# Kernel tuning notes

Hardware: AMD Instinct MI355X
Metric: run time of the kernel (lower is better)

## Reference

```python
import jax, jax.numpy as jnp
from jax import lax
import numpy as np

N_VOX = 50000
B = 2
D, H, W = 8, 160, 160
CIN = 16
G = 3
K = 27
CHANS = [(16, 16), (16, 32), (32, 64), (64, 64), (64, 128)]
NAMES = ['in', 'e1', 'e2', 'e3', 'out']


def setup_inputs() -> dict:
    key = jax.random.key(0)
    ks = jax.random.split(key, 16)
    rng = np.random.default_rng(0)
    # unique active cells -> deterministic scatter/gather rulebook
    lin = rng.choice(B * D * H * W, size=N_VOX, replace=False)
    bz = lin // (D * H * W)
    rem = lin % (D * H * W)
    zz = rem // (H * W)
    yy = (rem % (H * W)) // W
    xx = rem % W
    coors = jnp.asarray(np.stack([bz, zz, yy, xx], 1).astype(np.int32))
    inp = {
        'voxel_features': jax.random.normal(ks[0], (N_VOX, CIN), jnp.float32),
        'coors': coors,
        'batch_size': B,
    }
    i = 1
    for nm, (ci, co) in zip(NAMES, CHANS):
        k1, k2 = jax.random.split(ks[i]); i += 1
        inp['wb_' + nm] = jax.random.normal(k1, (K, ci, co), jnp.float32) * 0.05
        inp['ws_' + nm] = jax.random.normal(k2, (K, ci, G, co), jnp.float32) * 0.05
        inp['gm_' + nm] = jnp.ones((co,), jnp.float32)
        inp['bt_' + nm] = jnp.zeros((co,), jnp.float32)
    return inp


def _kan_block(feat, nbr, wb, ws, gm, bt, centers, inv_h):
    # submanifold KAN conv: gather -> (silu base + RBF spline basis) GEMM -> accumulate
    n = feat.shape[0]
    fp = jnp.concatenate([feat, jnp.zeros((1, feat.shape[1]), feat.dtype)], 0)  # pad row for out-of-grid

    def body(acc, kin):
        idx, wbk, wsk = kin
        x = fp[idx]                                   # [N, Cin] gathered neighbors
        base = jax.nn.silu(x) @ wbk                   # [N, Cout]
        bas = jnp.exp(-jnp.square((x[:, :, None] - centers) * inv_h))  # [N, Cin, G]
        spl = jnp.einsum('ncg,cgo->no', bas, wsk)     # [N, Cout]
        return acc + base + spl, None

    out0 = jnp.zeros((n, wb.shape[-1]), feat.dtype)
    out, _ = lax.scan(jax.checkpoint(body), out0, (nbr, wb, ws))
    # BatchNorm1d (train-mode batch stats) + ReLU
    mu = out.mean(0)
    var = out.var(0)
    out = (out - mu) * lax.rsqrt(var + 1e-3) * gm + bt
    return jax.nn.relu(out)


def _build_rulebook(coors, batch_size, n):
    grid = jnp.full((batch_size, D + 2, H + 2, W + 2), n, jnp.int32)
    grid = grid.at[coors[:, 0], coors[:, 1] + 1, coors[:, 2] + 1, coors[:, 3] + 1].set(
        jnp.arange(n, dtype=jnp.int32))
    offs = [(dz, dy, dx) for dz in (-1, 0, 1) for dy in (-1, 0, 1) for dx in (-1, 0, 1)]
    return jnp.stack([
        grid[coors[:, 0], coors[:, 1] + 1 + dz, coors[:, 2] + 1 + dy, coors[:, 3] + 1 + dx]
        for dz, dy, dx in offs])  # [27, N]


def reference(voxel_features, coors, batch_size,
              wb_in, ws_in, gm_in, bt_in,
              wb_e1, ws_e1, gm_e1, bt_e1,
              wb_e2, ws_e2, gm_e2, bt_e2,
              wb_e3, ws_e3, gm_e3, bt_e3,
              wb_out, ws_out, gm_out, bt_out):
    n = voxel_features.shape[0]
    nbr = _build_rulebook(coors, batch_size, n)
    centers = jnp.linspace(-1.0, 1.0, G)
    inv_h = (G - 1) / 2.0
    x = _kan_block(voxel_features, nbr, wb_in, ws_in, gm_in, bt_in, centers, inv_h)
    x = _kan_block(x, nbr, wb_e1, ws_e1, gm_e1, bt_e1, centers, inv_h)
    x = _kan_block(x, nbr, wb_e2, ws_e2, gm_e2, bt_e2, centers, inv_h)
    x = _kan_block(x, nbr, wb_e3, ws_e3, gm_e3, bt_e3, centers, inv_h)
    x = _kan_block(x, nbr, wb_out, ws_out, gm_out, bt_out, centers, inv_h)
    co = x.shape[1]
    dense = jnp.zeros((batch_size, D, H, W, co), x.dtype)
    dense = dense.at[coors[:, 0], coors[:, 1], coors[:, 2], coors[:, 3]].set(x)
    dense = dense.transpose(0, 4, 1, 2, 3)            # [B, C, D, H, W]
    return dense.reshape(batch_size, co * D, H, W)    # [B, C*D, H, W]
```

## Files before the change

### kernel.cpp

```cpp
#include <hip/hip_runtime.h>

#define N_VOX 50000
#define BATCH 2
#define DD 8
#define HH 160
#define WW 160
#define PD 10
#define PH 162
#define PW 162
#define KK 27
#define NCELL (BATCH*DD*HH*WW)
#define GRID_ELEMS (BATCH*PD*PH*PW)
#define OUT_ELEMS (BATCH*128*DD*HH*WW)

typedef __attribute__((ext_vector_type(8))) short short8v;
typedef __attribute__((ext_vector_type(4))) float float4v;

__device__ inline unsigned short f2bf(float f) {
    unsigned u = __float_as_uint(f);
    u += 0x7FFFu + ((u >> 16) & 1u);
    return (unsigned short)(u >> 16);
}

__global__ void k_flags(const int* __restrict__ coors, int* __restrict__ flags) {
    int n = blockIdx.x * 256 + threadIdx.x;
    if (n >= N_VOX) return;
    int b = coors[n*4+0], z = coors[n*4+1], y = coors[n*4+2], x = coors[n*4+3];
    flags[((b*DD + z)*HH + y)*WW + x] = 1;
}

__global__ void k_scan1(const int* __restrict__ flags, int* __restrict__ scanout,
                        int* __restrict__ bsums) {
    __shared__ int s[256];
    int t = threadIdx.x, blk = blockIdx.x;
    int4 v = ((const int4*)(flags + blk*1024))[t];
    int tsum = v.x + v.y + v.z + v.w;
    s[t] = tsum; __syncthreads();
    for (int off = 1; off < 256; off <<= 1) {
        int x = (t >= off) ? s[t-off] : 0;
        __syncthreads(); s[t] += x; __syncthreads();
    }
    int excl = s[t] - tsum;
    int4 o; o.x = excl; o.y = excl + v.x; o.z = o.y + v.y; o.w = o.z + v.z;
    ((int4*)(scanout + blk*1024))[t] = o;
    if (t == 255) bsums[blk] = s[255];
}

__global__ void k_scan2(int* __restrict__ bsums) {
    __shared__ int s[512];
    int t = threadIdx.x;
    int orig = (t < 400) ? bsums[t] : 0;
    s[t] = orig; __syncthreads();
    for (int off = 1; off < 512; off <<= 1) {
        int x = (t >= off) ? s[t-off] : 0;
        __syncthreads(); s[t] += x; __syncthreads();
    }
    if (t < 400) bsums[t] = s[t] - orig;
}

__global__ void k_pos(const int* __restrict__ coors, const int* __restrict__ scanout,
                      const int* __restrict__ bsums, int* __restrict__ pos_of,
                      int* __restrict__ vox_at) {
    int n = blockIdx.x * 256 + threadIdx.x;
    if (n >= N_VOX) return;
    int b = coors[n*4+0], z = coors[n*4+1], y = coors[n*4+2], x = coors[n*4+3];
    int lin = ((b*DD + z)*HH + y)*WW + x;
    int pos = scanout[lin] + bsums[lin >> 10];
    pos_of[n] = pos;
    vox_at[pos] = n;
}

__global__ void k_gridP(const int* __restrict__ coors, const int* __restrict__ pos_of,
                        int* __restrict__ gridP) {
    int n = blockIdx.x * 256 + threadIdx.x;
    if (n >= N_VOX) return;
    int b = coors[n*4+0], z = coors[n*4+1], y = coors[n*4+2], x = coors[n*4+3];
    gridP[((b*PD + z+1)*PH + (y+1))*PW + (x+1)] = pos_of[n];
}

__global__ void k_nbrP(const int* __restrict__ coors, const int* __restrict__ vox_at,
                       const int* __restrict__ gridP, int* __restrict__ nbrP) {
    int i = blockIdx.x * 256 + threadIdx.x;
    if (i >= N_VOX) return;
    int n = vox_at[i];
    int b = coors[n*4+0], z = coors[n*4+1]+1, y = coors[n*4+2]+1, x = coors[n*4+3]+1;
    int k = 0;
    for (int dz = -1; dz <= 1; ++dz)
        for (int dy = -1; dy <= 1; ++dy)
            for (int dx = -1; dx <= 1; ++dx) {
                int g = gridP[((b*PD + z+dz)*PH + (y+dy))*PW + (x+dx)];
                nbrP[k*N_VOX + i] = (g >= 0) ? g : N_VOX;
                ++k;
            }
}

__global__ void k_phi0(const float* __restrict__ vf, const int* __restrict__ vox_at,
                       unsigned short* __restrict__ phi) {
    int e = blockIdx.x * 256 + threadIdx.x;
    if (e >= (N_VOX + 1) * 16) return;
    int i = e / 16, c = e % 16;
    float x = 0.f;
    if (i < N_VOX) x = vf[(size_t)vox_at[i] * 16 + c];
    float sig = 1.f / (1.f + __expf(-x));
    ushort4 p;
    p.x = f2bf(x * sig);
    p.y = f2bf(__expf(-(x + 1.f) * (x + 1.f)));
    p.z = f2bf(__expf(-x * x));
    p.w = f2bf(__expf(-(x - 1.f) * (x - 1.f)));
    *(ushort4*)&phi[(size_t)e * 4] = p;
}

struct WswzArgs {
    const float* wb[5];
    const float* ws[5];
    unsigned short* dst[5];
};
__global__ void k_wswz_all(WswzArgs a) {
    constexpr int off[6]   = {0, 27648, 82944, 304128, 746496, 1631232};
    constexpr int lgCI4[5] = {6, 6, 7, 8, 8};
    constexpr int lgCO[5]  = {4, 5, 6, 6, 7};
    int e = blockIdx.x * 256 + threadIdx.x;
    if (e >= off[5]) return;
    int L = 0;
    #pragma unroll
    for (int i = 1; i < 5; ++i) L += (e >= off[i]);
    int el = e - off[L];
    int CIN4 = 1 << lgCI4[L], COUT = 1 << lgCO[L], CIN = CIN4 >> 2;
    int j8   = el & 7;
    int rest = el >> 3;
    int o    = rest & (COUT - 1);
    int kb   = rest >> lgCO[L];
    int kabs = kb * 8 + j8;
    int k  = kabs >> lgCI4[L];
    int c4 = kabs & (CIN4 - 1);
    int c = c4 >> 2, jj = c4 & 3;
    float v = (jj == 0) ? a.wb[L][(k * CIN + c) * COUT + o]
                        : a.ws[L][((k * CIN + c) * 3 + (jj - 1)) * COUT + o];
    a.dst[L][el] = f2bf(v);
}

template<int CIN, int COUT, int NSPL>
__global__ __launch_bounds__(64, 2) void k_conv_mfma(
    const unsigned short* __restrict__ phi,
    const int*            __restrict__ nbrP,
    const unsigned short* __restrict__ Wsw,
    float*                __restrict__ pre,
    float*                __restrict__ sums)
{
    constexpr int CIN4   = CIN * 4;
    constexpr int BK     = 64;
    constexpr int SPK    = CIN4 / BK;
    constexpr int NSTAGE = KK * SPK;
    constexpr int COUTH  = COUT / NSPL;
    constexpr int NFW    = COUTH / 16;
    constexpr int WR     = 4;
    constexpr int NMB    = (N_VOX + 63) / 64;
    constexpr int NBLK   = NMB * NSPL;
    constexpr int PERX   = (NBLK + 7) / 8;

    int lb = blockIdx.x;
    int linear = (lb & 7) * PERX + (lb >> 3);
    if (linear >= NBLK) return;
    const int mb = linear / NSPL, h = linear % NSPL;

    const int lane = threadIdx.x & 63;
    const int l15 = lane & 15, q = lane >> 4;
    const int base = mb * 64;
    int vg[WR];
    #pragma unroll
    for (int rs = 0; rs < WR; ++rs) vg[rs] = base + rs * 16 + l15;
    const int ob = h * COUTH;

    const unsigned short* bp = Wsw + (size_t)(q * COUT + ob + l15) * 8;

    int rows[WR], rowsN[WR];
    short8v A0[2][WR], A1[2][WR];
    short8v B0[2][NFW], B1[2][NFW];

    auto loadB = [&](int sp, short8v (&Bb)[2][NFW]) {
        #pragma unroll
        for (int kk = 0; kk < 2; ++kk)
            #pragma unroll
            for (int nf = 0; nf < NFW; ++nf)
                Bb[kk][nf] = *(const short8v*)(bp +
                    ((size_t)(sp * 8 + kk * 4) * COUT + nf * 16) * 8);
    };
    auto loadA = [&](int sp, short8v (&Ab)[2][WR]) {
        if (sp % SPK == 0) {
            #pragma unroll
            for (int rs = 0; rs < WR; ++rs) rows[rs] = rowsN[rs];
        }
        const int c4s = (sp % SPK) * BK;
        #pragma unroll
        for (int rs = 0; rs < WR; ++rs) {
            const unsigned short* p = phi + (size_t)rows[rs] * CIN4 + c4s + q * 8;
            Ab[0][rs] = *(const short8v*)p;
            Ab[1][rs] = *(const short8v*)(p + 32);
        }
        if (sp % SPK == 0) {
            int k2 = sp / SPK + 1;
            if (k2 < KK) {
                #pragma unroll
                for (int rs = 0; rs < WR; ++rs)
                    rowsN[rs] = (vg[rs] < N_VOX) ? nbrP[k2 * N_VOX + vg[rs]] : N_VOX;
            }
        }
    };

    float4v acc[WR][NFW];
    #pragma unroll
    for (int rs = 0; rs < WR; ++rs)
        #pragma unroll
        for (int nf = 0; nf < NFW; ++nf)
            acc[rs][nf] = (float4v){0.f, 0.f, 0.f, 0.f};

    auto domfma = [&](const short8v (&Ab)[2][WR], const short8v (&Bb)[2][NFW]) {
        #pragma unroll
        for (int kk = 0; kk < 2; ++kk)
            #pragma unroll
            for (int nf = 0; nf < NFW; ++nf)
                #pragma unroll
                for (int rs = 0; rs < WR; ++rs)
                    acc[rs][nf] = __builtin_amdgcn_mfma_f32_16x16x32_bf16(
                        Ab[kk][rs], Bb[kk][nf], acc[rs][nf], 0, 0, 0);
    };

    #pragma unroll
    for (int rs = 0; rs < WR; ++rs) {
        rows[rs]  = (vg[rs] < N_VOX) ? nbrP[vg[rs]] : N_VOX;
        rowsN[rs] = (vg[rs] < N_VOX) ? nbrP[N_VOX + vg[rs]] : N_VOX;
    }
    loadB(0, B0);
    #pragma unroll
    for (int rs = 0; rs < WR; ++rs) {
        const unsigned short* p = phi + (size_t)rows[rs] * CIN4 + q * 8;
        A0[0][rs] = *(const short8v*)p;
        A0[1][rs] = *(const short8v*)(p + 32);
    }

    #define SLOT(T, Ac, Bc, An, Bn)                                   \
        if ((T) + 1 < NSTAGE) { loadB((T) + 1, Bn); loadA((T) + 1, An); } \
        __builtin_amdgcn_sched_barrier(0);                            \
        domfma(Ac, Bc);

    int s = 0;
    for (; s + 2 <= NSTAGE; s += 2) {
        SLOT(s + 0, A0, B0, A1, B1)
        SLOT(s + 1, A1, B1, A0, B0)
    }
    if constexpr (NSTAGE % 2 != 0) {
        domfma(A0, B0);
    }
    #undef SLOT

    #pragma unroll
    for (int rs = 0; rs < WR; ++rs)
        #pragma unroll
        for (int nf = 0; nf < NFW; ++nf)
            #pragma unroll
            for (int r = 0; r < 4; ++r) {
                int v = base + rs * 16 + q * 4 + r;
                if (v < N_VOX)
                    pre[(size_t)v * COUT + ob + nf * 16 + l15] = acc[rs][nf][r];
            }

    float* S = sums + (blockIdx.x & 7) * 256;
    #pragma unroll
    for (int nf = 0; nf < NFW; ++nf) {
        float s1 = 0.f, s2 = 0.f;
        #pragma unroll
        for (int rs = 0; rs < WR; ++rs)
            #pragma unroll
            for (int r = 0; r < 4; ++r) {
                int v = base + rs * 16 + q * 4 + r;
                if (v < N_VOX) {
                    float a = acc[rs][nf][r];
                    s1 += a; s2 += a * a;
                }
            }
        s1 += __shfl_xor(s1, 16); s1 += __shfl_xor(s1, 32);
        s2 += __shfl_xor(s2, 16); s2 += __shfl_xor(s2, 32);
        if (q == 0) {
            atomicAdd(&S[ob + nf * 16 + l15], s1);
            atomicAdd(&S[COUT + ob + nf * 16 + l15], s2);
        }
    }
}

template<int COUT>
__global__ void k_bnapply_phi(const float* __restrict__ pre, const float* __restrict__ sums,
                              const float* __restrict__ gm, const float* __restrict__ bt,
                              unsigned short* __restrict__ phi) {
    __shared__ float sc[COUT], sh[COUT];
    int t = threadIdx.x;
    if (t < COUT) {
        float s1 = 0.f, s2 = 0.f;
        #pragma unroll
        for (int xo = 0; xo < 8; ++xo) {
            s1 += sums[xo * 256 + t];
            s2 += sums[xo * 256 + COUT + t];
        }
        float mu  = s1 * (1.f / N_VOX);
        float var = s2 * (1.f / N_VOX) - mu*mu;
        float s = rsqrtf(var + 1e-3f) * gm[t];
        sc[t] = s;
        sh[t] = bt[t] - mu * s;
    }
    __syncthreads();
    int tot = (N_VOX + 1) * COUT;
    for (int e = blockIdx.x*256 + t; e < tot; e += gridDim.x*256) {
        int i = e / COUT, c = e % COUT;
        float x = 0.f;
        if (i < N_VOX) x = fmaxf(pre[(size_t)i*COUT + c] * sc[c] + sh[c], 0.f);
        float sig = 1.f / (1.f + __expf(-x));
        ushort4 p;
        p.x = f2bf(x * sig);
        p.y = f2bf(__expf(-(x + 1.f) * (x + 1.f)));
        p.z = f2bf(__expf(-x * x));
        p.w = f2bf(__expf(-(x - 1.f) * (x - 1.f)));
        *(ushort4*)&phi[(size_t)e * 4] = p;
    }
}

template<int COUT>
__global__ void k_bnapply_f32(float* __restrict__ pre, const float* __restrict__ sums,
                              const float* __restrict__ gm, const float* __restrict__ bt) {
    __shared__ float sc[COUT], sh[COUT];
    int t = threadIdx.x;
    if (t < COUT) {
        float s1 = 0.f, s2 = 0.f;
        #pragma unroll
        for (int xo = 0; xo < 8; ++xo) {
            s1 += sums[xo * 256 + t];
            s2 += sums[xo * 256 + COUT + t];
        }
        float mu  = s1 * (1.f / N_VOX);
        float var = s2 * (1.f / N_VOX) - mu*mu;
        float s = rsqrtf(var + 1e-3f) * gm[t];
        sc[t] = s;
        sh[t] = bt[t] - mu * s;
    }
    __syncthreads();
    for (int e = blockIdx.x*256 + t; e < N_VOX*COUT; e += gridDim.x*256) {
        int c = e % COUT;
        pre[e] = fmaxf(pre[e] * sc[c] + sh[c], 0.f);
    }
}

__global__ void k_dense(const float* __restrict__ feat, const int* __restrict__ gridP,
                        float* __restrict__ out) {
    int e4 = blockIdx.x*256 + threadIdx.x;
    if (e4 >= OUT_ELEMS/4) return;
    int e = e4 * 4;
    int x  = e % WW;
    int y  = (e / WW) % HH;
    int cz = (e / (WW*HH)) % (128*DD);
    int b  = e / (WW*HH*128*DD);
    int c = cz >> 3, z = cz & 7;
    const int* gp = &gridP[((b*PD + z+1)*PH + (y+1))*PW + (x+1)];
    int g0 = gp[0], g1 = gp[1], g2 = gp[2], g3 = gp[3];
    float4 o;
    o.x = (g0 >= 0) ? feat[(size_t)g0*128 + c] : 0.f;
    o.y = (g1 >= 0) ? feat[(size_t)g1*128 + c] : 0.f;
    o.z = (g2 >= 0) ? feat[(size_t)g2*128 + c] : 0.f;
    o.w = (g3 >= 0) ? feat[(size_t)g3*128 + c] : 0.f;
    *(float4*)&out[e] = o;
}

template<int CIN, int COUT, int NSPL>
static void run_block(const float* gm, const float* bt,
                      const int* nbrP, unsigned short* phi, const unsigned short* Wsw,
                      float* sums, float* pre, bool last, hipStream_t stream) {
    constexpr int NMB  = (N_VOX + 63) / 64;
    constexpr int NBLK = NMB * NSPL;
    constexpr int GRID = ((NBLK + 7) / 8) * 8;
    k_conv_mfma<CIN, COUT, NSPL><<<GRID, 64, 0, stream>>>(phi, nbrP, Wsw, pre, sums);
    if (last) {
        k_bnapply_f32<COUT><<<512, 256, 0, stream>>>(pre, sums, gm, bt);
    } else {
        k_bnapply_phi<COUT><<<512, 256, 0, stream>>>(pre, sums, gm, bt, phi);
    }
}

extern "C" void kernel_launch(void* const* d_in, const int* in_sizes, int n_in,
                              void* d_out, int out_size, void* d_ws, size_t ws_size,
                              hipStream_t stream) {
    const float* vf    = (const float*)d_in[0];
    const int*   coors = (const int*)d_in[1];
    const float* wb[5] = {(const float*)d_in[3],  (const float*)d_in[7],
                          (const float*)d_in[11], (const float*)d_in[15],
                          (const float*)d_in[19]};
    const float* wsp[5]= {(const float*)d_in[4],  (const float*)d_in[8],
                          (const float*)d_in[12], (const float*)d_in[16],
                          (const float*)d_in[20]};
    const float* gm[5] = {(const float*)d_in[5],  (const float*)d_in[9],
                          (const float*)d_in[13], (const float*)d_in[17],
                          (const float*)d_in[21]};
    const float* bt[5] = {(const float*)d_in[6],  (const float*)d_in[10],
                          (const float*)d_in[14], (const float*)d_in[18],
                          (const float*)d_in[22]};

    char* p = (char*)d_ws;
    auto alloc = [&](size_t bytes) {
        char* r = p;
        p += (bytes + 255) & ~(size_t)255;
        return r;
    };
    int*            flags   = (int*)           alloc((size_t)NCELL * 4);
    int*            scanout = (int*)           alloc((size_t)NCELL * 4);
    int*            bsums   = (int*)           alloc(512 * 4);
    int*            pos_of  = (int*)           alloc((size_t)N_VOX * 4);
    int*            vox_at  = (int*)           alloc((size_t)N_VOX * 4);
    int*            gridP   = (int*)           alloc((size_t)GRID_ELEMS * 4);
    int*            nbrP    = (int*)           alloc((size_t)KK * N_VOX * 4);
    unsigned short* Wsw0    = (unsigned short*)alloc((size_t)KK * 64  * 16  * 2);
    unsigned short* Wsw1    = (unsigned short*)alloc((size_t)KK * 64  * 32  * 2);
    unsigned short* Wsw2    = (unsigned short*)alloc((size_t)KK * 128 * 64  * 2);
    unsigned short* Wsw3    = (unsigned short*)alloc((size_t)KK * 256 * 64  * 2);
    unsigned short* Wsw4    = (unsigned short*)alloc((size_t)KK * 256 * 128 * 2);
    unsigned short* phi     = (unsigned short*)alloc((size_t)(N_VOX + 1) * 256 * 2);
    float*          sumsAll = (float*)         alloc(5 * 8 * 256 * 4);
    float*          pre     = (float*)         alloc((size_t)N_VOX * 128 * 4);

    hipMemsetAsync(flags, 0, (size_t)NCELL * 4, stream);
    hipMemsetAsync(gridP, 0xFF, (size_t)GRID_ELEMS * 4, stream);
    hipMemsetAsync(sumsAll, 0, 5 * 8 * 256 * 4, stream);

    WswzArgs wa;
    for (int i = 0; i < 5; ++i) { wa.wb[i] = wb[i]; wa.ws[i] = wsp[i]; }
    wa.dst[0] = Wsw0; wa.dst[1] = Wsw1; wa.dst[2] = Wsw2; wa.dst[3] = Wsw3; wa.dst[4] = Wsw4;
    k_wswz_all<<<(1631232 + 255) / 256, 256, 0, stream>>>(wa);

    k_flags<<<(N_VOX+255)/256, 256, 0, stream>>>(coors, flags);
    k_scan1<<<NCELL/1024, 256, 0, stream>>>(flags, scanout, bsums);
    k_scan2<<<1, 512, 0, stream>>>(bsums);
    k_pos  <<<(N_VOX+255)/256, 256, 0, stream>>>(coors, scanout, bsums, pos_of, vox_at);
    k_gridP<<<(N_VOX+255)/256, 256, 0, stream>>>(coors, pos_of, gridP);
    k_nbrP <<<(N_VOX+255)/256, 256, 0, stream>>>(coors, vox_at, gridP, nbrP);
    {
        int n = (N_VOX + 1) * 16;
        k_phi0<<<(n + 255) / 256, 256, 0, stream>>>(vf, vox_at, phi);
    }

    run_block<16, 16,  1>(gm[0], bt[0], nbrP, phi, Wsw0, sumsAll + 0*2048, pre, false, stream);
    run_block<16, 32,  1>(gm[1], bt[1], nbrP, phi, Wsw1, sumsAll + 1*2048, pre, false, stream);
    run_block<32, 64,  1>(gm[2], bt[2], nbrP, phi, Wsw2, sumsAll + 2*2048, pre, false, stream);
    run_block<64, 64,  1>(gm[3], bt[3], nbrP, phi, Wsw3, sumsAll + 3*2048, pre, false, stream);
    run_block<64, 128, 2>(gm[4], bt[4], nbrP, phi, Wsw4, sumsAll + 4*2048, pre, true,  stream);

    k_dense<<<(OUT_ELEMS/4 + 255)/256, 256, 0, stream>>>(pre, gridP, (float*)d_out);
}
```

Baseline: 661.8 us.

## Add LDS-staged 4-wave MFMA conv kernel with direct global-to-LDS loads for wider layers

Adds a new conv kernel for the 32/64/128-channel layers. It uses 256-thread blocks covering 128 voxels and double-buffers the gathered activation rows and weight tiles in LDS with global_load_lds, so four waves share the weight tile. The previous single-wave kernel presumably loaded operands per wave with no sharing. The new kernel adds a block barrier per K-stage and a larger LDS footprint, which can limit occupancy.

```diff
diff --git a/kernel.cpp b/kernel.cpp
--- a/kernel.cpp
+++ b/kernel.cpp
@@ -20,6 +20,12 @@
     unsigned u = __float_as_uint(f);
     u += 0x7FFFu + ((u >> 16) & 1u);
     return (unsigned short)(u >> 16);
+}
+
+__device__ inline void gload_lds16(const void* g, void* l) {
+    __builtin_amdgcn_global_load_lds(
+        (const __attribute__((address_space(1))) void*)g,
+        (__attribute__((address_space(3))) void*)l, 16, 0, 0);
 }
 
 __global__ void k_flags(const int* __restrict__ coors, int* __restrict__ flags) {
@@ -287,6 +293,151 @@
     }
 }
 
+template<int CIN, int COUT>
+__global__ __launch_bounds__(256, 2) void k_conv_lds(
+    const unsigned short* __restrict__ phi,
+    const int*            __restrict__ nbrP,
+    const unsigned short* __restrict__ Wsw,
+    float*                __restrict__ pre,
+    float*                __restrict__ sums)
+{
+    constexpr int CIN4   = CIN * 4;
+    constexpr int BK     = 64;
+    constexpr int SPK    = CIN4 / BK;
+    constexpr int NSTAGE = KK * SPK;
+    constexpr int NFW    = COUT / 32;
+    constexpr int NMB    = (N_VOX + 127) / 128;
+    constexpr int PERX   = (NMB + 7) / 8;
+    constexpr int BENT   = 8 * COUT;
+    constexpr int NBI    = (BENT / 64) / 4;
+
+    __shared__ short8v lds[2 * 1024 + 2 * BENT];
+
+    int lb = blockIdx.x;
+    int mb = (lb & 7) * PERX + (lb >> 3);
+    if (mb >= NMB) return;
+
+    const int t = threadIdx.x, lane = t & 63, w = t >> 6;
+    const int l15 = lane & 15, q = lane >> 4;
+    const int wm = w >> 1, wn = w & 1;
+    const int base = mb * 128;
+    const int ob = wn * (COUT / 2);
+
+    short8v* ldsA = lds;
+    short8v* ldsB = lds + 2048;
+
+    auto nbrR = [&](int k, int j) -> int {
+        return (base + j < N_VOX) ? nbrP[k * N_VOX + base + j] : N_VOX;
+    };
+    int r0 = nbrR(0, lane), r1 = nbrR(0, 64 + lane);
+    int rn0 = nbrR(1, lane), rn1 = nbrR(1, 64 + lane);
+
+    auto stage = [&](int spn) {
+        const int nb = spn & 1;
+        const int cs = (spn % SPK) * BK;
+        #pragma unroll
+        for (int i = 0; i < 4; ++i) {
+            const int m = w * 4 + i;
+            const int c = m >> 1, half = m & 1;
+            const unsigned short* src =
+                phi + (size_t)(half ? r1 : r0) * CIN4 + cs + c * 8;
+            gload_lds16(src, ldsA + nb * 1024 + m * 64);
+        }
+        #pragma unroll
+        for (int i = 0; i < NBI; ++i) {
+            const int m = w * NBI + i;
+            const unsigned short* src =
+                Wsw + ((size_t)spn * BENT + m * 64 + lane) * 8;
+            gload_lds16(src, ldsB + nb * BENT + m * 64);
+        }
+    };
+
+    float4v acc[4][NFW];
+    #pragma unroll
+    for (int rs = 0; rs < 4; ++rs)
+        #pragma unroll
+        for (int nf = 0; nf < NFW; ++nf)
+            acc[rs][nf] = (float4v){0.f, 0.f, 0.f, 0.f};
+
+    stage(0);
+    asm volatile("s_waitcnt vmcnt(0)" ::: "memory");
+    __builtin_amdgcn_sched_barrier(0);
+    __builtin_amdgcn_s_barrier();
+    __builtin_amdgcn_sched_barrier(0);
+
+    for (int sp = 0; sp < NSTAGE; ++sp) {
+        const int spn = sp + 1;
+        if (spn < NSTAGE) {
+            if (spn % SPK == 0) {
+                r0 = rn0; r1 = rn1;
+                int k2 = spn / SPK + 1;
+                if (k2 < KK) { rn0 = nbrR(k2, lane); rn1 = nbrR(k2, 64 + lane); }
+            }
+            stage(spn);
+        }
+        __builtin_amdgcn_sched_barrier(0);
+        const short8v* A = ldsA + (sp & 1) * 1024 + wm * 64 + l15;
+        const short8v* B = ldsB + (sp & 1) * BENT + ob + l15;
+        short8v af[2][4], bf[2][NFW];
+        #pragma unroll
+        for (int kk = 0; kk < 2; ++kk) {
+            #pragma unroll
+            for (int rs = 0; rs < 4; ++rs)
+                af[kk][rs] = A[(kk * 4 + q) * 128 + rs * 16];
+            #pragma unroll
+            for (int nf = 0; nf < NFW; ++nf)
+                bf[kk][nf] = B[(kk * 4 + q) * COUT + nf * 16];
+        }
+        #pragma unroll
+        for (int kk = 0; kk < 2; ++kk)
+            #pragma unroll
+            for (int nf = 0; nf < NFW; ++nf)
+                #pragma unroll
+                for (int rs = 0; rs < 4; ++rs)
+                    acc[rs][nf] = __builtin_amdgcn_mfma_f32_16x16x32_bf16(
+                        af[kk][rs], bf[kk][nf], acc[rs][nf], 0, 0, 0);
+        if (spn < NSTAGE) {
+            asm volatile("s_waitcnt vmcnt(0)" ::: "memory");
+            __builtin_amdgcn_sched_barrier(0);
+            __builtin_amdgcn_s_barrier();
+            __builtin_amdgcn_sched_barrier(0);
+        }
+    }
+
+    #pragma unroll
+    for (int rs = 0; rs < 4; ++rs)
+        #pragma unroll
+        for (int nf = 0; nf < NFW; ++nf)
+            #pragma unroll
+            for (int r = 0; r < 4; ++r) {
+                int v = base + wm * 64 + rs * 16 + q * 4 + r;
+                if (v < N_VOX)
+                    pre[(size_t)v * COUT + ob + nf * 16 + l15] = acc[rs][nf][r];
+            }
+
+    float* S = sums + (blockIdx.x & 7) * 256;
+    #pragma unroll
+    for (int nf = 0; nf < NFW; ++nf) {
+        float s1 = 0.f, s2 = 0.f;
+        #pragma unroll
+        for (int rs = 0; rs < 4; ++rs)
+            #pragma unroll
+            for (int r = 0; r < 4; ++r) {
+                int v = base + wm * 64 + rs * 16 + q * 4 + r;
+                if (v < N_VOX) {
+                    float a = acc[rs][nf][r];
+                    s1 += a; s2 += a * a;
+                }
+            }
+        s1 += __shfl_xor(s1, 16); s1 += __shfl_xor(s1, 32);
+        s2 += __shfl_xor(s2, 16); s2 += __shfl_xor(s2, 32);
+        if (q == 0) {
+            atomicAdd(&S[ob + nf * 16 + l15], s1);
+            atomicAdd(&S[COUT + ob + nf * 16 + l15], s2);
+        }
+    }
+}
+
 template<int COUT>
 __global__ void k_bnapply_phi(const float* __restrict__ pre, const float* __restrict__ sums,
                               const float* __restrict__ gm, const float* __restrict__ bt,
@@ -375,6 +526,20 @@
     constexpr int NBLK = NMB * NSPL;
     constexpr int GRID = ((NBLK + 7) / 8) * 8;
     k_conv_mfma<CIN, COUT, NSPL><<<GRID, 64, 0, stream>>>(phi, nbrP, Wsw, pre, sums);
+    if (last) {
+        k_bnapply_f32<COUT><<<512, 256, 0, stream>>>(pre, sums, gm, bt);
+    } else {
+        k_bnapply_phi<COUT><<<512, 256, 0, stream>>>(pre, sums, gm, bt, phi);
+    }
+}
+
+template<int CIN, int COUT>
+static void run_block_lds(const float* gm, const float* bt,
+                          const int* nbrP, unsigned short* phi, const unsigned short* Wsw,
+                          float* sums, float* pre, bool last, hipStream_t stream) {
+    constexpr int NMB  = (N_VOX + 127) / 128;
+    constexpr int GRID = ((NMB + 7) / 8) * 8;
+    k_conv_lds<CIN, COUT><<<GRID, 256, 0, stream>>>(phi, nbrP, Wsw, pre, sums);
     if (last) {
         k_bnapply_f32<COUT><<<512, 256, 0, stream>>>(pre, sums, gm, bt);
     } else {
@@ -442,11 +607,11 @@
         k_phi0<<<(n + 255) / 256, 256, 0, stream>>>(vf, vox_at, phi);
     }
 
-    run_block<16, 16,  1>(gm[0], bt[0], nbrP, phi, Wsw0, sumsAll + 0*2048, pre, false, stream);
-    run_block<16, 32,  1>(gm[1], bt[1], nbrP, phi, Wsw1, sumsAll + 1*2048, pre, false, stream);
-    run_block<32, 64,  1>(gm[2], bt[2], nbrP, phi, Wsw2, sumsAll + 2*2048, pre, false, stream);
-    run_block<64, 64,  1>(gm[3], bt[3], nbrP, phi, Wsw3, sumsAll + 3*2048, pre, false, stream);
-    run_block<64, 128, 2>(gm[4], bt[4], nbrP, phi, Wsw4, sumsAll + 4*2048, pre, true,  stream);
+    run_block<16, 16, 1>(gm[0], bt[0], nbrP, phi, Wsw0, sumsAll + 0*2048, pre, false, stream);
+    run_block<16, 32, 1>(gm[1], bt[1], nbrP, phi, Wsw1, sumsAll + 1*2048, pre, false, stream);
+    run_block_lds<32, 64 >(gm[2], bt[2], nbrP, phi, Wsw2, sumsAll + 2*2048, pre, false, stream);
+    run_block_lds<64, 64 >(gm[3], bt[3], nbrP, phi, Wsw3, sumsAll + 3*2048, pre, false, stream);
+    run_block_lds<64, 128>(gm[4], bt[4], nbrP, phi, Wsw4, sumsAll + 4*2048, pre, true,  stream);
 
     k_dense<<<(OUT_ELEMS/4 + 255)/256, 256, 0, stream>>>(pre, gridP, (float*)d_out);
 }
```

Measured after the change: 661.8 us. About the same (+0.0%).

## Add sparse-neighbor conv kernel that skips empty offsets using precomputed zero-input constants

Applied to the files above, without the earlier changes.

Adds a new conv kernel for the three larger layers. Per offset it compacts only the valid neighbors with ballots into a list, runs MFMA on just those rows, and scatters the results into an LDS accumulator with atomics. Missing neighbors are not left as zero: the spline basis of a zero input is nonzero, so a precomputed per-offset constant (sum over the spline weights) is subtracted for each present neighbor and the total constant is added once. With 50k active cells in a 410k-cell grid most neighbors are empty, so this cuts the dense gather-GEMM work. The cost is LDS atomic contention, an extra weight-reduction kernel, and a larger LDS footprint per block.

```diff
diff --git a/kernel.cpp b/kernel.cpp
--- a/kernel.cpp
+++ b/kernel.cpp
@@ -137,6 +137,37 @@
     float v = (jj == 0) ? a.wb[L][(k * CIN + c) * COUT + o]
                         : a.ws[L][((k * CIN + c) * 3 + (jj - 1)) * COUT + o];
     a.dst[L][el] = f2bf(v);
+}
+
+struct CkArgs { const float* ws[3]; float* ck[3]; };
+__global__ void k_ck_all(CkArgs a) {
+    constexpr int off[4]   = {0, 1792, 3584, 7168};
+    constexpr int CINs[3]  = {32, 64, 64};
+    constexpr int COUTs[3] = {64, 64, 128};
+    const float EI = 0.36787944117144233f;
+    int e = blockIdx.x * 256 + threadIdx.x;
+    if (e >= off[3]) return;
+    int L = 0;
+    #pragma unroll
+    for (int i = 1; i < 3; ++i) L += (e >= off[i]);
+    int el = e - off[L];
+    int CIN = CINs[L], COUT = COUTs[L];
+    int k = el / COUT, col = el % COUT;
+    const float* ws = a.ws[L];
+    float s = 0.f;
+    if (k < 27) {
+        for (int c = 0; c < CIN; ++c) {
+            const float* p = ws + ((size_t)(k * CIN + c) * 3) * COUT + col;
+            s += EI * (p[0] + p[2 * COUT]) + p[COUT];
+        }
+    } else {
+        for (int kk = 0; kk < 27; ++kk)
+            for (int c = 0; c < CIN; ++c) {
+                const float* p = ws + ((size_t)(kk * CIN + c) * 3) * COUT + col;
+                s += EI * (p[0] + p[2 * COUT]) + p[COUT];
+            }
+    }
+    a.ck[L][el] = s;
 }
 
 template<int CIN, int COUT, int NSPL>
@@ -287,6 +318,116 @@
     }
 }
 
+template<int CIN, int COUT>
+__global__ __launch_bounds__(256, 2) void k_conv_sparse(
+    const unsigned short* __restrict__ phi,
+    const int*            __restrict__ nbrP,
+    const unsigned short* __restrict__ Wsw,
+    const float*          __restrict__ ck,
+    float*                __restrict__ pre,
+    float*                __restrict__ sums)
+{
+    constexpr int CIN4 = CIN * 4;
+    constexpr int KKN  = CIN4 / 32;
+    constexpr int STR  = COUT / 4;
+    constexpr int NFW  = STR / 16;
+    constexpr int NMB  = (N_VOX + 127) / 128;
+    constexpr int PERX = (NMB + 7) / 8;
+
+    __shared__ float accL[128 * COUT];
+    __shared__ int   listI[4][128];
+    __shared__ int   listR[4][128];
+
+    int lb = blockIdx.x;
+    int mb = (lb & 7) * PERX + (lb >> 3);
+    if (mb >= NMB) return;
+
+    const int t = threadIdx.x, lane = t & 63, w = t >> 6;
+    const int l15 = lane & 15, q = lane >> 4;
+    const int base = mb * 128;
+    const int ob = w * STR;
+
+    for (int e = t; e < 128 * COUT / 4; e += 256)
+        ((float4*)accL)[e] = make_float4(0.f, 0.f, 0.f, 0.f);
+    __syncthreads();
+
+    const unsigned long long lt = (1ull << lane) - 1;
+    const int ja = base + lane, jb = ja + 64;
+
+    for (int k = 0; k < KK; ++k) {
+        int rA = (ja < N_VOX) ? nbrP[k * N_VOX + ja] : N_VOX;
+        int rB = (jb < N_VOX) ? nbrP[k * N_VOX + jb] : N_VOX;
+        bool pA = rA < N_VOX, pB = rB < N_VOX;
+        unsigned long long mA = __ballot(pA), mB = __ballot(pB);
+        int cA = __popcll(mA);
+        int rk = cA + __popcll(mB);
+        if (rk == 0) continue;
+        if (pA) { int p0 = __popcll(mA & lt);      listI[w][p0] = rA; listR[w][p0] = lane;      }
+        if (pB) { int p1 = cA + __popcll(mB & lt); listI[w][p1] = rB; listR[w][p1] = 64 + lane; }
+
+        short8v bf[KKN][NFW];
+        #pragma unroll
+        for (int kk = 0; kk < KKN; ++kk)
+            #pragma unroll
+            for (int nf = 0; nf < NFW; ++nf)
+                bf[kk][nf] = *(const short8v*)(Wsw +
+                    (size_t)((k * (CIN4 / 8) + kk * 4 + q) * COUT + ob + nf * 16 + l15) * 8);
+        float ckv[NFW];
+        #pragma unroll
+        for (int nf = 0; nf < NFW; ++nf)
+            ckv[nf] = ck[k * COUT + ob + nf * 16 + l15];
+
+        int nrt = (rk + 15) >> 4;
+        for (int rt = 0; rt < nrt; ++rt) {
+            int pos = rt * 16 + l15;
+            int in  = (pos < rk) ? listI[w][pos] : N_VOX;
+            const unsigned short* pa = phi + (size_t)in * CIN4 + q * 8;
+            short8v af[KKN];
+            #pragma unroll
+            for (int kk = 0; kk < KKN; ++kk)
+                af[kk] = *(const short8v*)(pa + kk * 32);
+            float4v accf[NFW];
+            #pragma unroll
+            for (int nf = 0; nf < NFW; ++nf) accf[nf] = (float4v){0.f, 0.f, 0.f, 0.f};
+            #pragma unroll
+            for (int kk = 0; kk < KKN; ++kk)
+                #pragma unroll
+                for (int nf = 0; nf < NFW; ++nf)
+                    accf[nf] = __builtin_amdgcn_mfma_f32_16x16x32_bf16(
+                        af[kk], bf[kk][nf], accf[nf], 0, 0, 0);
+            #pragma unroll
+            for (int r = 0; r < 4; ++r) {
+                int p2 = rt * 16 + q * 4 + r;
+                if (p2 < rk) {
+                    int lr = listR[w][p2];
+                    #pragma unroll
+                    for (int nf = 0; nf < NFW; ++nf)
+                        atomicAdd(&accL[lr * COUT + ob + nf * 16 + l15],
+                                  accf[nf][r] - ckv[nf]);
+                }
+            }
+        }
+    }
+    __syncthreads();
+
+    const int col = t & (COUT - 1);
+    constexpr int RSTEP = 256 / COUT;
+    const int r0w = t / COUT;
+    float Ct = ck[27 * COUT + col];
+    float s1 = 0.f, s2 = 0.f;
+    for (int row = r0w; row < 128; row += RSTEP) {
+        int v = base + row;
+        if (v < N_VOX) {
+            float val = accL[row * COUT + col] + Ct;
+            pre[(size_t)v * COUT + col] = val;
+            s1 += val; s2 += val * val;
+        }
+    }
+    float* S = sums + (blockIdx.x & 7) * 256;
+    atomicAdd(&S[col], s1);
+    atomicAdd(&S[COUT + col], s2);
+}
+
 template<int COUT>
 __global__ void k_bnapply_phi(const float* __restrict__ pre, const float* __restrict__ sums,
                               const float* __restrict__ gm, const float* __restrict__ bt,
@@ -375,6 +516,21 @@
     constexpr int NBLK = NMB * NSPL;
     constexpr int GRID = ((NBLK + 7) / 8) * 8;
     k_conv_mfma<CIN, COUT, NSPL><<<GRID, 64, 0, stream>>>(phi, nbrP, Wsw, pre, sums);
+    if (last) {
+        k_bnapply_f32<COUT><<<512, 256, 0, stream>>>(pre, sums, gm, bt);
+    } else {
+        k_bnapply_phi<COUT><<<512, 256, 0, stream>>>(pre, sums, gm, bt, phi);
+    }
+}
+
+template<int CIN, int COUT>
+static void run_block_sparse(const float* gm, const float* bt,
+                             const int* nbrP, unsigned short* phi, const unsigned short* Wsw,
+                             const float* ck, float* sums, float* pre, bool last,
+                             hipStream_t stream) {
+    constexpr int NMB  = (N_VOX + 127) / 128;
+    constexpr int GRID = ((NMB + 7) / 8) * 8;
+    k_conv_sparse<CIN, COUT><<<GRID, 256, 0, stream>>>(phi, nbrP, Wsw, ck, pre, sums);
     if (last) {
         k_bnapply_f32<COUT><<<512, 256, 0, stream>>>(pre, sums, gm, bt);
     } else {
@@ -421,6 +577,7 @@
     unsigned short* phi     = (unsigned short*)alloc((size_t)(N_VOX + 1) * 256 * 2);
     float*          sumsAll = (float*)         alloc(5 * 8 * 256 * 4);
     float*          pre     = (float*)         alloc((size_t)N_VOX * 128 * 4);
+    float*          ckAll   = (float*)         alloc(7168 * 4);
 
     hipMemsetAsync(flags, 0, (size_t)NCELL * 4, stream);
     hipMemsetAsync(gridP, 0xFF, (size_t)GRID_ELEMS * 4, stream);
@@ -430,6 +587,11 @@
     for (int i = 0; i < 5; ++i) { wa.wb[i] = wb[i]; wa.ws[i] = wsp[i]; }
     wa.dst[0] = Wsw0; wa.dst[1] = Wsw1; wa.dst[2] = Wsw2; wa.dst[3] = Wsw3; wa.dst[4] = Wsw4;
     k_wswz_all<<<(1631232 + 255) / 256, 256, 0, stream>>>(wa);
+
+    CkArgs ca;
+    ca.ws[0] = wsp[2]; ca.ws[1] = wsp[3]; ca.ws[2] = wsp[4];
+    ca.ck[0] = ckAll;  ca.ck[1] = ckAll + 1792; ca.ck[2] = ckAll + 3584;
+    k_ck_all<<<(7168 + 255) / 256, 256, 0, stream>>>(ca);
 
     k_flags<<<(N_VOX+255)/256, 256, 0, stream>>>(coors, flags);
     k_scan1<<<NCELL/1024, 256, 0, stream>>>(flags, scanout, bsums);
@@ -442,11 +604,11 @@
         k_phi0<<<(n + 255) / 256, 256, 0, stream>>>(vf, vox_at, phi);
     }
 
-    run_block<16, 16,  1>(gm[0], bt[0], nbrP, phi, Wsw0, sumsAll + 0*2048, pre, false, stream);
-    run_block<16, 32,  1>(gm[1], bt[1], nbrP, phi, Wsw1, sumsAll + 1*2048, pre, false, stream);
-    run_block<32, 64,  1>(gm[2], bt[2], nbrP, phi, Wsw2, sumsAll + 2*2048, pre, false, stream);
-    run_block<64, 64,  1>(gm[3], bt[3], nbrP, phi, Wsw3, sumsAll + 3*2048, pre, false, stream);
-    run_block<64, 128, 2>(gm[4], bt[4], nbrP, phi, Wsw4, sumsAll + 4*2048, pre, true,  stream);
+    run_block<16, 16, 1>(gm[0], bt[0], nbrP, phi, Wsw0, sumsAll + 0*2048, pre, false, stream);
+    run_block<16, 32, 1>(gm[1], bt[1], nbrP, phi, Wsw1, sumsAll + 1*2048, pre, false, stream);
+    run_block_sparse<32, 64 >(gm[2], bt[2], nbrP, phi, Wsw2, ckAll,        sumsAll + 2*2048, pre, false, stream);
+    run_block_sparse<64, 64 >(gm[3], bt[3], nbrP, phi, Wsw3, ckAll + 1792, sumsAll + 3*2048, pre, false, stream);
+    run_block_sparse<64, 128>(gm[4], bt[4], nbrP, phi, Wsw4, ckAll + 3584, sumsAll + 4*2048, pre, true,  stream);
 
     k_dense<<<(OUT_ELEMS/4 + 255)/256, 256, 0, stream>>>(pre, gridP, (float*)d_out);
 }
```

New measurement: 1.296 ms. 95.9% more time.
